# Kernel tuning notes

Measured on AMD Instinct MI355X. Metric: run time of the kernel, lower is better.

## Reference

```python
import jax, jax.numpy as jnp
import numpy as np

EPS = 1e-5  # eqx.nn.LayerNorm default


def _layer_norm(x, w, b):
    m = x.mean(-1, keepdims=True)
    v = ((x - m) ** 2).mean(-1, keepdims=True)
    return (x - m) / jnp.sqrt(v + EPS) * w + b


def _s4_block(x, nw, nb, lre, lim, bre, bim, cre, cim, d, lstep, ow, ob, o2w, o2b):
    # x: [L, H]. One SequenceBlock: LayerNorm -> S4 recurrence (lax.scan) -> GELU -> GLU-style gated linear -> residual.
    skip = x
    h = _layer_norm(x, nw, nb)
    Lam = lre + 1j * lim                      # [H, N] complex diagonal state matrix
    step = jnp.exp(lstep)[:, None]            # [H, 1] per-channel timescale
    BL = 1.0 / (1.0 - (step / 2.0) * Lam)     # bilinear discretization
    Abar = BL * (1.0 + (step / 2.0) * Lam)    # [H, N]
    Bbar = BL * step * (bre + 1j * bim)       # [H, N]
    C = cre + 1j * cim                        # [H, N]

    def scan_fn(state, u):                    # state: [H, N] complex, u: [H]
        new = Abar * state + Bbar * u[:, None]
        y = 2.0 * jnp.sum(C * new, axis=-1).real + d * u
        return new, y

    init = jnp.zeros(Abar.shape, Abar.dtype)  # cell.init_state
    _, y = jax.lax.scan(scan_fn, init, h)     # [L, H]
    y = jax.nn.gelu(y)
    y = (y @ ow.T + ob) * jax.nn.sigmoid(y @ o2w.T + o2b)
    return skip + y


def setup_inputs() -> dict:
    key = jax.random.key(0)
    L, IN, OUT, H, N, NL = 2048, 4, 3, 512, 32, 4
    ks = jax.random.split(key, 16)
    return {
        "x": jax.random.normal(ks[0], (L, IN), jnp.float32),
        "enc_w": jax.random.normal(ks[1], (H, IN), jnp.float32) / np.sqrt(IN),
        "enc_b": jnp.zeros((H,), jnp.float32),
        "dec_w": jax.random.normal(ks[2], (OUT, H), jnp.float32) / np.sqrt(H),
        "dec_b": jnp.zeros((OUT,), jnp.float32),
        "norm_w": jnp.ones((NL, H), jnp.float32),
        "norm_b": jnp.zeros((NL, H), jnp.float32),
        "lam_re": -0.5 - jax.random.uniform(ks[3], (NL, H, N), jnp.float32),  # stable (Re < 0)
        "lam_im": np.pi * jax.random.normal(ks[4], (NL, H, N), jnp.float32),
        "b_re": jax.random.normal(ks[5], (NL, H, N), jnp.float32) / np.sqrt(N),
        "b_im": jax.random.normal(ks[6], (NL, H, N), jnp.float32) / np.sqrt(N),
        "c_re": jax.random.normal(ks[7], (NL, H, N), jnp.float32) / np.sqrt(N),
        "c_im": jax.random.normal(ks[8], (NL, H, N), jnp.float32) / np.sqrt(N),
        "d": jax.random.normal(ks[9], (NL, H), jnp.float32),
        "log_step": float(np.log(1e-3)) + float(np.log(1e-1) - np.log(1e-3)) * jax.random.uniform(ks[10], (NL, H), jnp.float32),
        "out_w": jax.random.normal(ks[11], (NL, H, H), jnp.float32) / np.sqrt(H),
        "out_b": jnp.zeros((NL, H), jnp.float32),
        "out2_w": jax.random.normal(ks[12], (NL, H, H), jnp.float32) / np.sqrt(H),
        "out2_b": jnp.zeros((NL, H), jnp.float32),
    }


def reference(x, enc_w, enc_b, dec_w, dec_b, norm_w, norm_b, lam_re, lam_im, b_re, b_im, c_re, c_im, d, log_step, out_w, out_b, out2_w, out2_b):
    h = x @ enc_w.T + enc_b                   # encoder: [L, IN] -> [L, H]
    for i in range(norm_w.shape[0]):          # fixed small n_layers loop
        h = _s4_block(h, norm_w[i], norm_b[i], lam_re[i], lam_im[i], b_re[i], b_im[i],
                      c_re[i], c_im[i], d[i], log_step[i], out_w[i], out_b[i], out2_w[i], out2_b[i])
    return h @ dec_w.T + dec_b                # decoder: [L, H] -> [L, OUT]
```

## Files before the change

kernel.cpp:

```cpp
#include <hip/hip_runtime.h>
#include <hip/hip_bf16.h>
#include <math.h>

#define LSEQ 2048
#define HD   512
#define NST  32
#define LC   16
#define NCHK 128
#define HH   (HD * HD)

typedef __bf16 bf16;
typedef __bf16 bf16x8 __attribute__((ext_vector_type(8)));
typedef float  floatx4 __attribute__((ext_vector_type(4)));

__device__ __forceinline__ float wave_reduce_add(float v) {
#pragma unroll
    for (int m = 32; m; m >>= 1) v += __shfl_xor(v, m, 64);
    return v;
}

__device__ __forceinline__ float gelu_tanh(float x) {
    float z = 0.7978845608028654f * (x + 0.044715f * x * x * x);
    float e = __expf(2.f * z);
    float th = 1.f - 2.f / (e + 1.f);
    return 0.5f * x * (1.f + th);
}

__device__ __forceinline__ void make_ab(float lre, float lim, float step,
                                        float br0, float bi0,
                                        float& ar, float& ai, float& br, float& bi) {
    float s2 = 0.5f * step;
    float dr = 1.f - s2 * lre, di = -s2 * lim;
    float inv = 1.f / (dr * dr + di * di);
    float blr = dr * inv, bli = -di * inv;
    float nr = 1.f + s2 * lre, ni = s2 * lim;
    ar = blr * nr - bli * ni;
    ai = blr * ni + bli * nr;
    float tr = step * br0, ti = step * bi0;
    br = blr * tr - bli * ti;
    bi = blr * ti + bli * tr;
}

__global__ __launch_bounds__(256) void prep_kernel(
    const float* __restrict__ lre, const float* __restrict__ lim,
    const float* __restrict__ bre, const float* __restrict__ bim,
    const float* __restrict__ cre, const float* __restrict__ cim,
    const float* __restrict__ ls,
    float2* __restrict__ cA, float2* __restrict__ cB,
    float2* __restrict__ cC, float2* __restrict__ cAp) {
    int tid = blockIdx.x * 256 + threadIdx.x;
    int lay = tid >> 14, rem = tid & 16383;
    int ch = rem >> 5, n = rem & 31;
    int src = tid;
    float step = __expf(ls[lay * HD + ch]);
    float ar, ai, br, bi;
    make_ab(lre[src], lim[src], step, bre[src], bim[src], ar, ai, br, bi);
    float xr = ar, xi = ai;
#pragma unroll
    for (int q = 0; q < 4; ++q) { float tt = xr * xr - xi * xi; xi = 2.f * xr * xi; xr = tt; }
    int dst = (lay * NST + n) * HD + ch;
    cA[dst]  = make_float2(ar, ai);
    cB[dst]  = make_float2(br, bi);
    cC[dst]  = make_float2(2.f * cre[src], 2.f * cim[src]);
    cAp[dst] = make_float2(xr, xi);
}

__global__ __launch_bounds__(256) void cvt_kernel(
    const float* __restrict__ ow, const float* __restrict__ o2w,
    bf16* __restrict__ wb) {
    const float* src = blockIdx.y ? o2w : ow;
    bf16* dst = wb + blockIdx.y * (4 * HH);
    int i = (blockIdx.x * 256 + threadIdx.x) * 8;
    float4 a = *(const float4*)(src + i);
    float4 b = *(const float4*)(src + i + 4);
    bf16x8 o;
    o[0] = (bf16)a.x; o[1] = (bf16)a.y; o[2] = (bf16)a.z; o[3] = (bf16)a.w;
    o[4] = (bf16)b.x; o[5] = (bf16)b.y; o[6] = (bf16)b.z; o[7] = (bf16)b.w;
    *(bf16x8*)(dst + i) = o;
}

__global__ __launch_bounds__(256) void enc_kernel(
    const float* __restrict__ x, const float* __restrict__ w,
    const float* __restrict__ b, float* __restrict__ h) {
    int idx = blockIdx.x * 256 + threadIdx.x;
    int t = idx >> 9, i = idx & (HD - 1);
    float acc = b[i];
    float4 xv = *(const float4*)(x + t * 4);
    float4 wv = *(const float4*)(w + i * 4);
    acc = fmaf(xv.x, wv.x, acc);
    acc = fmaf(xv.y, wv.y, acc);
    acc = fmaf(xv.z, wv.z, acc);
    acc = fmaf(xv.w, wv.w, acc);
    h[idx] = acc;
}

__global__ __launch_bounds__(256) void ln_kernel(
    const float* __restrict__ h, float* __restrict__ hn,
    const float* __restrict__ w, const float* __restrict__ b) {
    int wv = threadIdx.x >> 6, lane = threadIdx.x & 63;
    int row = blockIdx.x * 4 + wv;
    const float* hp = h + row * HD + lane * 8;
    float v[8];
    *(float4*)(v)     = *(const float4*)(hp);
    *(float4*)(v + 4) = *(const float4*)(hp + 4);
    float s = 0.f;
#pragma unroll
    for (int e = 0; e < 8; ++e) s += v[e];
    s = wave_reduce_add(s);
    float m = s * (1.f / HD);
    float q = 0.f;
#pragma unroll
    for (int e = 0; e < 8; ++e) { float d = v[e] - m; q += d * d; }
    q = wave_reduce_add(q);
    float rstd = rsqrtf(q * (1.f / HD) + 1e-5f);
    float w8[8], b8[8];
    *(float4*)(w8)     = *(const float4*)(w + lane * 8);
    *(float4*)(w8 + 4) = *(const float4*)(w + lane * 8 + 4);
    *(float4*)(b8)     = *(const float4*)(b + lane * 8);
    *(float4*)(b8 + 4) = *(const float4*)(b + lane * 8 + 4);
    float o[8];
#pragma unroll
    for (int e = 0; e < 8; ++e)
        o[e] = (v[e] - m) * rstd * w8[e] + b8[e];
    float* op = hn + row * HD + lane * 8;
    *(float4*)op       = *(float4*)o;
    *(float4*)(op + 4) = *(float4*)(o + 4);
}

__global__ __launch_bounds__(256, 1) void p1_kernel(
    const float* __restrict__ u,
    const float2* __restrict__ cA, const float2* __restrict__ cB,
    float2* __restrict__ f, int lay) {
    int lane = threadIdx.x & 63, w = threadIdx.x >> 6;
    int ch = blockIdx.x * 32 + (lane & 31);
    int sub = lane >> 5;
    int chunk = blockIdx.y * 4 + w;
    int cbase = (lay * NST + sub * 16) * HD + ch;
    float aR[16], aI[16], bR[16], bI[16];
#pragma unroll
    for (int j = 0; j < 16; ++j) {
        float2 t = cA[cbase + j * HD]; aR[j] = t.x; aI[j] = t.y;
        t = cB[cbase + j * HD];        bR[j] = t.x; bI[j] = t.y;
    }
    float sr[16], si[16];
#pragma unroll
    for (int j = 0; j < 16; ++j) { sr[j] = 0.f; si[j] = 0.f; }
    const float* up = u + chunk * LC * HD + ch;
#pragma unroll 4
    for (int t = 0; t < LC; ++t) {
        float uu = up[t * HD];
#pragma unroll
        for (int j = 0; j < 16; ++j) {
            float nr = fmaf(aR[j], sr[j], fmaf(-aI[j], si[j], bR[j] * uu));
            float ni = fmaf(aI[j], sr[j], fmaf( aR[j], si[j], bI[j] * uu));
            sr[j] = nr; si[j] = ni;
        }
    }
    float2* fp = f + (chunk * NST + sub * 16) * HD + ch;
#pragma unroll
    for (int j = 0; j < 16; ++j) fp[j * HD] = make_float2(sr[j], si[j]);
}

__global__ __launch_bounds__(64, 1) void p2_kernel(
    float2* __restrict__ f, const float2* __restrict__ cAp, int lay) {
    int ch = blockIdx.x * 64 + threadIdx.x;
    int n = blockIdx.y;
    float2 ap = cAp[(lay * NST + n) * HD + ch];
    float sr = 0.f, si = 0.f;
    float2* fp = f + n * HD + ch;
#pragma unroll 4
    for (int c = 0; c < NCHK; ++c) {
        float2 v = fp[(size_t)c * NST * HD];
        float nr = fmaf(ap.x, sr, fmaf(-ap.y, si, v.x));
        float ni = fmaf(ap.y, sr, fmaf( ap.x, si, v.y));
        sr = nr; si = ni;
        fp[(size_t)c * NST * HD] = make_float2(sr, si);
    }
}

__global__ __launch_bounds__(256, 1) void p3_kernel(
    const float* __restrict__ u, const float2* __restrict__ f,
    const float2* __restrict__ cA, const float2* __restrict__ cB,
    const float2* __restrict__ cC, const float* __restrict__ d_p,
    bf16* __restrict__ g, int lay) {
    int lane = threadIdx.x & 63, w = threadIdx.x >> 6;
    int ch = blockIdx.x * 32 + (lane & 31);
    int sub = lane >> 5;
    int chunk = blockIdx.y * 4 + w;
    int cbase = (lay * NST + sub * 16) * HD + ch;
    float aR[16], aI[16], bR[16], bI[16], cR[16], cI[16];
#pragma unroll
    for (int j = 0; j < 16; ++j) {
        float2 t = cA[cbase + j * HD]; aR[j] = t.x; aI[j] = t.y;
        t = cB[cbase + j * HD];        bR[j] = t.x; bI[j] = t.y;
        t = cC[cbase + j * HD];        cR[j] = t.x; cI[j] = t.y;
    }
    float dch = d_p[lay * HD + ch];
    float sr[16], si[16];
    if (chunk > 0) {
        const float2* ip = f + ((chunk - 1) * NST + sub * 16) * HD + ch;
#pragma unroll
        for (int j = 0; j < 16; ++j) { float2 v = ip[j * HD]; sr[j] = v.x; si[j] = v.y; }
    } else {
#pragma unroll
        for (int j = 0; j < 16; ++j) { sr[j] = 0.f; si[j] = 0.f; }
    }
    const float* up = u + chunk * LC * HD + ch;
    bf16* gp = g + chunk * LC * HD + ch;
#pragma unroll 4
    for (int t = 0; t < LC; ++t) {
        float uu = up[t * HD];
        float p = 0.f;
#pragma unroll
        for (int j = 0; j < 16; ++j) {
            float nr = fmaf(aR[j], sr[j], fmaf(-aI[j], si[j], bR[j] * uu));
            float ni = fmaf(aI[j], sr[j], fmaf( aR[j], si[j], bI[j] * uu));
            sr[j] = nr; si[j] = ni;
            p = fmaf(cR[j], nr, fmaf(-cI[j], ni, p));
        }
        p += __shfl_xor(p, 32);
        float y = fmaf(dch, uu, p);
        if (sub == 0) gp[t * HD] = (bf16)gelu_tanh(y);
    }
}

__global__ __launch_bounds__(256) void mm_kernel(
    const bf16* __restrict__ A,
    const bf16* __restrict__ W1,
    const bf16* __restrict__ W2,
    const float* __restrict__ bias1, const float* __restrict__ bias2,
    float* __restrict__ Hio) {
    const int w = threadIdx.x >> 6, lane = threadIdx.x & 63;
    const int wm = w >> 1, wn = w & 1;
    const int mBase = blockIdx.y * 64 + wm * 32;
    const int nBase = blockIdx.x * 64 + wn * 32;
    const int lrow = lane & 15, quad = lane >> 4;

    floatx4 acc1[2][2] = {{{0.f,0.f,0.f,0.f},{0.f,0.f,0.f,0.f}},{{0.f,0.f,0.f,0.f},{0.f,0.f,0.f,0.f}}};
    floatx4 acc2[2][2] = {{{0.f,0.f,0.f,0.f},{0.f,0.f,0.f,0.f}},{{0.f,0.f,0.f,0.f},{0.f,0.f,0.f,0.f}}};

    for (int k0 = 0; k0 < HD; k0 += 32) {
        int kk = k0 + quad * 8;
        bf16x8 a0 = *(const bf16x8*)(A + (mBase + lrow) * HD + kk);
        bf16x8 a1 = *(const bf16x8*)(A + (mBase + 16 + lrow) * HD + kk);
        bf16x8 p0 = *(const bf16x8*)(W1 + (nBase + lrow) * HD + kk);
        bf16x8 p1 = *(const bf16x8*)(W1 + (nBase + 16 + lrow) * HD + kk);
        bf16x8 q0 = *(const bf16x8*)(W2 + (nBase + lrow) * HD + kk);
        bf16x8 q1 = *(const bf16x8*)(W2 + (nBase + 16 + lrow) * HD + kk);
        acc1[0][0] = __builtin_amdgcn_mfma_f32_16x16x32_bf16(a0, p0, acc1[0][0], 0, 0, 0);
        acc1[0][1] = __builtin_amdgcn_mfma_f32_16x16x32_bf16(a0, p1, acc1[0][1], 0, 0, 0);
        acc1[1][0] = __builtin_amdgcn_mfma_f32_16x16x32_bf16(a1, p0, acc1[1][0], 0, 0, 0);
        acc1[1][1] = __builtin_amdgcn_mfma_f32_16x16x32_bf16(a1, p1, acc1[1][1], 0, 0, 0);
        acc2[0][0] = __builtin_amdgcn_mfma_f32_16x16x32_bf16(a0, q0, acc2[0][0], 0, 0, 0);
        acc2[0][1] = __builtin_amdgcn_mfma_f32_16x16x32_bf16(a0, q1, acc2[0][1], 0, 0, 0);
        acc2[1][0] = __builtin_amdgcn_mfma_f32_16x16x32_bf16(a1, q0, acc2[1][0], 0, 0, 0);
        acc2[1][1] = __builtin_amdgcn_mfma_f32_16x16x32_bf16(a1, q1, acc2[1][1], 0, 0, 0);
    }

#pragma unroll
    for (int fm = 0; fm < 2; ++fm)
#pragma unroll
        for (int fn = 0; fn < 2; ++fn) {
            int j = nBase + fn * 16 + lrow;
            float bb1 = bias1[j], bb2 = bias2[j];
#pragma unroll
            for (int r = 0; r < 4; ++r) {
                int t = mBase + fm * 16 + quad * 4 + r;
                float z1 = acc1[fm][fn][r] + bb1;
                float z2 = acc2[fm][fn][r] + bb2;
                float val = z1 / (1.f + __expf(-z2));
                Hio[t * HD + j] += val;
            }
        }
}

__global__ __launch_bounds__(192) void dec_kernel(
    const float* __restrict__ h, const float* __restrict__ w,
    const float* __restrict__ b, float* __restrict__ out) {
    int j = threadIdx.x >> 6, lane = threadIdx.x & 63;
    int t = blockIdx.x;
    const float* hp = h + t * HD + lane * 8;
    float v[8];
    *(float4*)(v)     = *(const float4*)(hp);
    *(float4*)(v + 4) = *(const float4*)(hp + 4);
    float w8[8];
    *(float4*)(w8)     = *(const float4*)(w + j * HD + lane * 8);
    *(float4*)(w8 + 4) = *(const float4*)(w + j * HD + lane * 8 + 4);
    float s = 0.f;
#pragma unroll
    for (int e = 0; e < 8; ++e) s = fmaf(v[e], w8[e], s);
    s = wave_reduce_add(s);
    if (lane == 0) out[t * 3 + j] = s + b[j];
}

extern "C" void kernel_launch(void* const* d_in, const int* in_sizes, int n_in,
                              void* d_out, int out_size, void* d_ws, size_t ws_size,
                              hipStream_t stream) {
    const float* x   = (const float*)d_in[0];
    const float* ew  = (const float*)d_in[1];
    const float* eb  = (const float*)d_in[2];
    const float* dw  = (const float*)d_in[3];
    const float* db  = (const float*)d_in[4];
    const float* nw  = (const float*)d_in[5];
    const float* nb  = (const float*)d_in[6];
    const float* lre = (const float*)d_in[7];
    const float* lim = (const float*)d_in[8];
    const float* bre = (const float*)d_in[9];
    const float* bim = (const float*)d_in[10];
    const float* cre = (const float*)d_in[11];
    const float* cim = (const float*)d_in[12];
    const float* dd  = (const float*)d_in[13];
    const float* ls  = (const float*)d_in[14];
    const float* ow  = (const float*)d_in[15];
    const float* ob  = (const float*)d_in[16];
    const float* o2w = (const float*)d_in[17];
    const float* o2b = (const float*)d_in[18];

    char* ws = (char*)d_ws;
    float*  h   = (float*)ws;
    float*  hn  = (float*)(ws + (4  << 20));
    float2* f   = (float2*)(ws + (8  << 20));
    bf16*   g   = (bf16*)(ws + (24 << 20));
    bf16*   wb  = (bf16*)(ws + (26 << 20));
    float2* cA  = (float2*)(ws + (30 << 20));
    float2* cB  = (float2*)(ws + (30 << 20) + (512 << 10));
    float2* cC  = (float2*)(ws + (31 << 20));
    float2* cAp = (float2*)(ws + (31 << 20) + (512 << 10));

    prep_kernel<<<256, 256, 0, stream>>>(lre, lim, bre, bim, cre, cim, ls, cA, cB, cC, cAp);
    cvt_kernel<<<dim3(4 * HH / (256 * 8), 2), 256, 0, stream>>>(ow, o2w, wb);
    enc_kernel<<<LSEQ * HD / 256, 256, 0, stream>>>(x, ew, eb, h);
    for (int lay = 0; lay < 4; ++lay) {
        int oH = lay * HD;
        ln_kernel<<<LSEQ / 4, 256, 0, stream>>>(h, hn, nw + oH, nb + oH);
        p1_kernel<<<dim3(HD / 32, NCHK / 4), 256, 0, stream>>>(hn, cA, cB, f, lay);
        p2_kernel<<<dim3(HD / 64, NST), 64, 0, stream>>>(f, cAp, lay);
        p3_kernel<<<dim3(HD / 32, NCHK / 4), 256, 0, stream>>>(hn, f, cA, cB, cC, dd, g, lay);
        mm_kernel<<<dim3(HD / 64, LSEQ / 64), 256, 0, stream>>>(
            g, wb + lay * HH, wb + 4 * HH + lay * HH, ob + oH, o2b + oH, h);
    }
    dec_kernel<<<LSEQ, 192, 0, stream>>>(h, dw, db, (float*)d_out);
}
```

Measured before the change: 351.0 us.

## Split chunk-carry scan into hierarchical three-pass scan and halve per-thread state

The serial 128-step cross-chunk carry scan is replaced by a three-level scan: local scans within 16-chunk superchunks, a short 8-step scan across superchunk ends using A^16 computed by repeated squaring, and a fixup pass that propagates carries with incrementally computed powers of A. Separately, the per-chunk kernels now give each thread 8 states instead of 16, with 4 lanes per channel and an extra shuffle reduction. This doubles the thread count and lowers register pressure, allowing higher occupancy. The cost is two extra kernel launches per layer, more global traffic over the f buffer, and slightly different floating-point rounding from the power-based carry.

```diff
diff --git a/kernel.cpp b/kernel.cpp
--- a/kernel.cpp
+++ b/kernel.cpp
@@ -7,6 +7,8 @@
 #define NST  32
 #define LC   16
 #define NCHK 128
+#define SUP  16
+#define NSUP 8
 #define HH   (HD * HD)
 
 typedef __bf16 bf16;
@@ -127,83 +129,129 @@
     *(float4*)(op + 4) = *(float4*)(o + 4);
 }
 
-__global__ __launch_bounds__(256, 1) void p1_kernel(
+__global__ __launch_bounds__(256, 4) void p1_kernel(
     const float* __restrict__ u,
     const float2* __restrict__ cA, const float2* __restrict__ cB,
     float2* __restrict__ f, int lay) {
     int lane = threadIdx.x & 63, w = threadIdx.x >> 6;
-    int ch = blockIdx.x * 32 + (lane & 31);
-    int sub = lane >> 5;
+    int ch = blockIdx.x * 16 + (lane & 15);
+    int sub = lane >> 4;
     int chunk = blockIdx.y * 4 + w;
-    int cbase = (lay * NST + sub * 16) * HD + ch;
-    float aR[16], aI[16], bR[16], bI[16];
-#pragma unroll
-    for (int j = 0; j < 16; ++j) {
+    int cbase = (lay * NST + sub * 8) * HD + ch;
+    float aR[8], aI[8], bR[8], bI[8];
+#pragma unroll
+    for (int j = 0; j < 8; ++j) {
         float2 t = cA[cbase + j * HD]; aR[j] = t.x; aI[j] = t.y;
         t = cB[cbase + j * HD];        bR[j] = t.x; bI[j] = t.y;
     }
-    float sr[16], si[16];
-#pragma unroll
-    for (int j = 0; j < 16; ++j) { sr[j] = 0.f; si[j] = 0.f; }
+    float sr[8], si[8];
+#pragma unroll
+    for (int j = 0; j < 8; ++j) { sr[j] = 0.f; si[j] = 0.f; }
     const float* up = u + chunk * LC * HD + ch;
 #pragma unroll 4
     for (int t = 0; t < LC; ++t) {
         float uu = up[t * HD];
 #pragma unroll
-        for (int j = 0; j < 16; ++j) {
+        for (int j = 0; j < 8; ++j) {
             float nr = fmaf(aR[j], sr[j], fmaf(-aI[j], si[j], bR[j] * uu));
             float ni = fmaf(aI[j], sr[j], fmaf( aR[j], si[j], bI[j] * uu));
             sr[j] = nr; si[j] = ni;
         }
     }
-    float2* fp = f + (chunk * NST + sub * 16) * HD + ch;
-#pragma unroll
-    for (int j = 0; j < 16; ++j) fp[j * HD] = make_float2(sr[j], si[j]);
-}
-
-__global__ __launch_bounds__(64, 1) void p2_kernel(
+    float2* fp = f + (chunk * NST + sub * 8) * HD + ch;
+#pragma unroll
+    for (int j = 0; j < 8; ++j) fp[j * HD] = make_float2(sr[j], si[j]);
+}
+
+__global__ __launch_bounds__(256) void p2a_kernel(
     float2* __restrict__ f, const float2* __restrict__ cAp, int lay) {
-    int ch = blockIdx.x * 64 + threadIdx.x;
-    int n = blockIdx.y;
+    int tg = blockIdx.x * 256 + threadIdx.x;
+    int ch = tg & 511;
+    int ns = tg >> 9;
+    int n = ns & 31, sup = ns >> 5;
     float2 ap = cAp[(lay * NST + n) * HD + ch];
+    float2* fp = f + ((sup * SUP) * NST + n) * HD + ch;
     float sr = 0.f, si = 0.f;
-    float2* fp = f + n * HD + ch;
 #pragma unroll 4
-    for (int c = 0; c < NCHK; ++c) {
-        float2 v = fp[(size_t)c * NST * HD];
+    for (int j = 0; j < SUP; ++j) {
+        float2 v = fp[(size_t)j * NST * HD];
         float nr = fmaf(ap.x, sr, fmaf(-ap.y, si, v.x));
         float ni = fmaf(ap.y, sr, fmaf( ap.x, si, v.y));
         sr = nr; si = ni;
-        fp[(size_t)c * NST * HD] = make_float2(sr, si);
-    }
-}
-
-__global__ __launch_bounds__(256, 1) void p3_kernel(
+        fp[(size_t)j * NST * HD] = make_float2(sr, si);
+    }
+}
+
+__global__ __launch_bounds__(256) void p2b_kernel(
+    float2* __restrict__ f, const float2* __restrict__ cAp, int lay) {
+    int tg = blockIdx.x * 256 + threadIdx.x;
+    int ch = tg & 511, n = tg >> 9;
+    float2 ap = cAp[(lay * NST + n) * HD + ch];
+    float xr = ap.x, xi = ap.y;
+#pragma unroll
+    for (int q = 0; q < 4; ++q) { float tt = xr * xr - xi * xi; xi = 2.f * xr * xi; xr = tt; }
+    float2* fp = f + ((SUP - 1) * NST + n) * HD + ch;
+    const size_t stride = (size_t)SUP * NST * HD;
+    float sr = 0.f, si = 0.f;
+#pragma unroll
+    for (int k = 0; k < NSUP; ++k) {
+        float2 v = fp[k * stride];
+        float nr = fmaf(xr, sr, fmaf(-xi, si, v.x));
+        float ni = fmaf(xi, sr, fmaf( xr, si, v.y));
+        sr = nr; si = ni;
+        fp[k * stride] = make_float2(sr, si);
+    }
+}
+
+__global__ __launch_bounds__(256) void p2c_kernel(
+    float2* __restrict__ f, const float2* __restrict__ cAp, int lay) {
+    int tg = blockIdx.x * 256 + threadIdx.x;
+    int ch = tg & 511;
+    int ns = tg >> 9;
+    int n = ns & 31, sup = ns >> 5;
+    if (sup == 0) return;
+    float2 ap = cAp[(lay * NST + n) * HD + ch];
+    float2 S = f[((sup * SUP - 1) * NST + n) * HD + ch];
+    float2* fp = f + ((sup * SUP) * NST + n) * HD + ch;
+    float wr = ap.x, wi = ap.y;
+#pragma unroll 4
+    for (int j = 0; j < SUP - 1; ++j) {
+        float2 v = fp[(size_t)j * NST * HD];
+        v.x += wr * S.x - wi * S.y;
+        v.y += wr * S.y + wi * S.x;
+        fp[(size_t)j * NST * HD] = v;
+        float nwr = wr * ap.x - wi * ap.y;
+        float nwi = wr * ap.y + wi * ap.x;
+        wr = nwr; wi = nwi;
+    }
+}
+
+__global__ __launch_bounds__(256, 3) void p3_kernel(
     const float* __restrict__ u, const float2* __restrict__ f,
     const float2* __restrict__ cA, const float2* __restrict__ cB,
     const float2* __restrict__ cC, const float* __restrict__ d_p,
     bf16* __restrict__ g, int lay) {
     int lane = threadIdx.x & 63, w = threadIdx.x >> 6;
-    int ch = blockIdx.x * 32 + (lane & 31);
-    int sub = lane >> 5;
+    int ch = blockIdx.x * 16 + (lane & 15);
+    int sub = lane >> 4;
     int chunk = blockIdx.y * 4 + w;
-    int cbase = (lay * NST + sub * 16) * HD + ch;
-    float aR[16], aI[16], bR[16], bI[16], cR[16], cI[16];
-#pragma unroll
-    for (int j = 0; j < 16; ++j) {
+    int cbase = (lay * NST + sub * 8) * HD + ch;
+    float aR[8], aI[8], bR[8], bI[8], cR[8], cI[8];
+#pragma unroll
+    for (int j = 0; j < 8; ++j) {
         float2 t = cA[cbase + j * HD]; aR[j] = t.x; aI[j] = t.y;
         t = cB[cbase + j * HD];        bR[j] = t.x; bI[j] = t.y;
         t = cC[cbase + j * HD];        cR[j] = t.x; cI[j] = t.y;
     }
     float dch = d_p[lay * HD + ch];
-    float sr[16], si[16];
+    float sr[8], si[8];
     if (chunk > 0) {
-        const float2* ip = f + ((chunk - 1) * NST + sub * 16) * HD + ch;
-#pragma unroll
-        for (int j = 0; j < 16; ++j) { float2 v = ip[j * HD]; sr[j] = v.x; si[j] = v.y; }
+        const float2* ip = f + ((chunk - 1) * NST + sub * 8) * HD + ch;
+#pragma unroll
+        for (int j = 0; j < 8; ++j) { float2 v = ip[j * HD]; sr[j] = v.x; si[j] = v.y; }
     } else {
 #pragma unroll
-        for (int j = 0; j < 16; ++j) { sr[j] = 0.f; si[j] = 0.f; }
+        for (int j = 0; j < 8; ++j) { sr[j] = 0.f; si[j] = 0.f; }
     }
     const float* up = u + chunk * LC * HD + ch;
     bf16* gp = g + chunk * LC * HD + ch;
@@ -212,12 +260,13 @@
         float uu = up[t * HD];
         float p = 0.f;
 #pragma unroll
-        for (int j = 0; j < 16; ++j) {
+        for (int j = 0; j < 8; ++j) {
             float nr = fmaf(aR[j], sr[j], fmaf(-aI[j], si[j], bR[j] * uu));
             float ni = fmaf(aI[j], sr[j], fmaf( aR[j], si[j], bI[j] * uu));
             sr[j] = nr; si[j] = ni;
             p = fmaf(cR[j], nr, fmaf(-cI[j], ni, p));
         }
+        p += __shfl_xor(p, 16);
         p += __shfl_xor(p, 32);
         float y = fmaf(dch, uu, p);
         if (sub == 0) gp[t * HD] = (bf16)gelu_tanh(y);
@@ -333,9 +382,11 @@
     for (int lay = 0; lay < 4; ++lay) {
         int oH = lay * HD;
         ln_kernel<<<LSEQ / 4, 256, 0, stream>>>(h, hn, nw + oH, nb + oH);
-        p1_kernel<<<dim3(HD / 32, NCHK / 4), 256, 0, stream>>>(hn, cA, cB, f, lay);
-        p2_kernel<<<dim3(HD / 64, NST), 64, 0, stream>>>(f, cAp, lay);
-        p3_kernel<<<dim3(HD / 32, NCHK / 4), 256, 0, stream>>>(hn, f, cA, cB, cC, dd, g, lay);
+        p1_kernel<<<dim3(HD / 16, NCHK / 4), 256, 0, stream>>>(hn, cA, cB, f, lay);
+        p2a_kernel<<<512, 256, 0, stream>>>(f, cAp, lay);
+        p2b_kernel<<<64, 256, 0, stream>>>(f, cAp, lay);
+        p2c_kernel<<<512, 256, 0, stream>>>(f, cAp, lay);
+        p3_kernel<<<dim3(HD / 16, NCHK / 4), 256, 0, stream>>>(hn, f, cA, cB, cC, dd, g, lay);
         mm_kernel<<<dim3(HD / 64, LSEQ / 64), 256, 0, stream>>>(
             g, wb + lay * HH, wb + 4 * HH + lay * HH, ob + oH, o2b + oH, h);
     }
```

Result: faster. 343.1 us (-2.2%).
